# Kernel tuning notes

Measured on AMD Instinct MI355X. Metric: run time of the kernel, lower is better.

Reference implementation:

```python
import jax, jax.numpy as jnp
import numpy as np

N = 16777216  # batch size

def setup_inputs() -> dict:
    key = jax.random.key(0)
    k1, k2 = jax.random.split(key)
    output = jax.random.normal(k1, (N, 2), dtype=jnp.float32)
    target = jax.random.randint(k2, (N,), 0, 2, dtype=jnp.int64)
    return {"output": output, "target": target}

def reference(output, target):
    # x_t[i] = output[i, 0] if target[i]==0 else output[i, 1]
    # equivalent to gathering output[i, target[i]] for binary targets
    x_t = jnp.take_along_axis(output, target[:, None].astype(jnp.int32), axis=1)  # [N,1]
    return jnp.mean((1.0 - x_t) ** 2)
```

## Files before the change

### kernel.cpp

```cpp
#include <hip/hip_runtime.h>
#include <hip/hip_bf16.h>


#define N_TOTAL 16777216
#define BLOCK 256
#define F4_PER_THREAD 8
#define F4_PER_BLOCK (BLOCK * F4_PER_THREAD)
#define N_F4 (N_TOTAL / 2)
#define GRID (N_F4 / F4_PER_BLOCK)

typedef float vfloat4 __attribute__((ext_vector_type(4)));
typedef int   vint2   __attribute__((ext_vector_type(2)));

__global__ __launch_bounds__(BLOCK) void floss_partial_kernel(
    const vfloat4* __restrict__ out4,
    const vint2*  __restrict__ tgt2,
    float* __restrict__ partials)
{
    const int t = threadIdx.x;
    const int vb = (blockIdx.x * 1365) & (GRID - 1);
    const int pbase = vb * F4_PER_BLOCK;

    vfloat4 f[F4_PER_THREAD];
    vint2   g[F4_PER_THREAD];

    #pragma unroll
    for (int j = 0; j < F4_PER_THREAD; ++j) {
        const int p = pbase + j * BLOCK + t;
        f[j] = __builtin_nontemporal_load(&out4[p]);
        g[j] = __builtin_nontemporal_load(&tgt2[p]);
    }

    float acc = 0.0f;
    #pragma unroll
    for (int j = 0; j < F4_PER_THREAD; ++j) {
        float x0 = g[j].x ? f[j].y : f[j].x;
        float x1 = g[j].y ? f[j].w : f[j].z;
        float d0 = 1.0f - x0, d1 = 1.0f - x1;
        acc += d0 * d0 + d1 * d1;
    }

    #pragma unroll
    for (int off = 32; off > 0; off >>= 1)
        acc += __shfl_down(acc, off, 64);

    __shared__ float smem[BLOCK / 64];
    const int lane = threadIdx.x & 63;
    const int wave = threadIdx.x >> 6;
    if (lane == 0) smem[wave] = acc;
    __syncthreads();

    if (threadIdx.x == 0) {
        float s = 0.0f;
        #pragma unroll
        for (int w = 0; w < BLOCK / 64; ++w) s += smem[w];
        partials[blockIdx.x] = s;
    }
}

__global__ __launch_bounds__(BLOCK) void floss_final_kernel(
    const vfloat4* __restrict__ partials4,
    float* __restrict__ result)
{
    const int t = threadIdx.x;
    float acc = 0.0f;
    #pragma unroll
    for (int j = 0; j < GRID / 4 / BLOCK; ++j) {
        vfloat4 p = partials4[j * BLOCK + t];
        acc += p.x + p.y + p.z + p.w;
    }

    #pragma unroll
    for (int off = 32; off > 0; off >>= 1)
        acc += __shfl_down(acc, off, 64);

    __shared__ float smem[BLOCK / 64];
    const int lane = threadIdx.x & 63;
    const int wave = threadIdx.x >> 6;
    if (lane == 0) smem[wave] = acc;
    __syncthreads();

    if (threadIdx.x == 0) {
        float s = 0.0f;
        #pragma unroll
        for (int w = 0; w < BLOCK / 64; ++w) s += smem[w];
        *result = s * (1.0f / (float)N_TOTAL);
    }
}

extern "C" void kernel_launch(void* const* d_in, const int* in_sizes, int n_in,
                              void* d_out, int out_size, void* d_ws, size_t ws_size,
                              hipStream_t stream) {
    const vfloat4* out4 = (const vfloat4*)d_in[0];
    const vint2*   tgt2 = (const vint2*)d_in[1];
    float* partials = (float*)d_ws;
    float* result = (float*)d_out;

    floss_partial_kernel<<<GRID, BLOCK, 0, stream>>>(out4, tgt2, partials);
    floss_final_kernel<<<1, BLOCK, 0, stream>>>((const vfloat4*)partials, result);
}
```

Before: 212.5 us.

## Fuse final reduction into main kernel via last-block atomic counter

Replaces the separate single-block final reduction kernel with a last-block-done pattern. Each block writes its partial, fences, and increments an atomic counter, and the last block sums all partials. It also drops the scrambled block-index mapping in favour of linear block order. This saves a kernel launch but adds a memset, fences and atomics, and changes the memory access order.

```diff
diff --git a/kernel.cpp b/kernel.cpp
--- a/kernel.cpp
+++ b/kernel.cpp
@@ -12,14 +12,15 @@
 typedef float vfloat4 __attribute__((ext_vector_type(4)));
 typedef int   vint2   __attribute__((ext_vector_type(2)));
 
-__global__ __launch_bounds__(BLOCK) void floss_partial_kernel(
+__global__ __launch_bounds__(BLOCK) void floss_kernel(
     const vfloat4* __restrict__ out4,
     const vint2*  __restrict__ tgt2,
-    float* __restrict__ partials)
+    unsigned int* __restrict__ counter,
+    float* __restrict__ partials,
+    float* __restrict__ result)
 {
     const int t = threadIdx.x;
-    const int vb = (blockIdx.x * 1365) & (GRID - 1);
-    const int pbase = vb * F4_PER_BLOCK;
+    const int pbase = blockIdx.x * F4_PER_BLOCK;
 
     vfloat4 f[F4_PER_THREAD];
     vint2   g[F4_PER_THREAD];
@@ -45,6 +46,7 @@
         acc += __shfl_down(acc, off, 64);
 
     __shared__ float smem[BLOCK / 64];
+    __shared__ bool amLast;
     const int lane = threadIdx.x & 63;
     const int wave = threadIdx.x >> 6;
     if (lane == 0) smem[wave] = acc;
@@ -55,36 +57,31 @@
         #pragma unroll
         for (int w = 0; w < BLOCK / 64; ++w) s += smem[w];
         partials[blockIdx.x] = s;
+        __threadfence();
+        unsigned int prev = atomicAdd(counter, 1u);
+        amLast = (prev == GRID - 1);
     }
-}
-
-__global__ __launch_bounds__(BLOCK) void floss_final_kernel(
-    const vfloat4* __restrict__ partials4,
-    float* __restrict__ result)
-{
-    const int t = threadIdx.x;
-    float acc = 0.0f;
-    #pragma unroll
-    for (int j = 0; j < GRID / 4 / BLOCK; ++j) {
-        vfloat4 p = partials4[j * BLOCK + t];
-        acc += p.x + p.y + p.z + p.w;
-    }
-
-    #pragma unroll
-    for (int off = 32; off > 0; off >>= 1)
-        acc += __shfl_down(acc, off, 64);
-
-    __shared__ float smem[BLOCK / 64];
-    const int lane = threadIdx.x & 63;
-    const int wave = threadIdx.x >> 6;
-    if (lane == 0) smem[wave] = acc;
     __syncthreads();
 
-    if (threadIdx.x == 0) {
-        float s = 0.0f;
+    if (amLast) {
+        __threadfence();
+        float a2 = 0.0f;
         #pragma unroll
-        for (int w = 0; w < BLOCK / 64; ++w) s += smem[w];
-        *result = s * (1.0f / (float)N_TOTAL);
+        for (int j = 0; j < GRID / BLOCK; ++j)
+            a2 += partials[j * BLOCK + t];
+
+        #pragma unroll
+        for (int off = 32; off > 0; off >>= 1)
+            a2 += __shfl_down(a2, off, 64);
+
+        if (lane == 0) smem[wave] = a2;
+        __syncthreads();
+        if (threadIdx.x == 0) {
+            float s = 0.0f;
+            #pragma unroll
+            for (int w = 0; w < BLOCK / 64; ++w) s += smem[w];
+            *result = s * (1.0f / (float)N_TOTAL);
+        }
     }
 }
 
@@ -93,9 +90,10 @@
                               hipStream_t stream) {
     const vfloat4* out4 = (const vfloat4*)d_in[0];
     const vint2*   tgt2 = (const vint2*)d_in[1];
-    float* partials = (float*)d_ws;
+    unsigned int* counter  = (unsigned int*)d_ws;
+    float*        partials = (float*)((char*)d_ws + 256);
     float* result = (float*)d_out;
 
-    floss_partial_kernel<<<GRID, BLOCK, 0, stream>>>(out4, tgt2, partials);
-    floss_final_kernel<<<1, BLOCK, 0, stream>>>((const vfloat4*)partials, result);
+    hipMemsetAsync(d_ws, 0, 4, stream);
+    floss_kernel<<<GRID, BLOCK, 0, stream>>>(out4, tgt2, counter, partials, result);
 }
```

Measured after the change: 414.3 us. +95.0%, slower.
